# Performance work log

Hardware: AMD Instinct MI355X
Metric: run time of the kernel (lower is better)

## Reference

```python
import jax, jax.numpy as jnp
import numpy as np
from jax import lax

LATENT, HIDDEN, OUT = 64, 128, 64
B, T = 4096, 100


def setup_inputs() -> dict:
    key = jax.random.key(0)
    ks = jax.random.split(key, 12)
    s = lambda fan_in: 1.0 / np.sqrt(fan_in)
    u = lambda k, shape, fan_in: jax.random.uniform(k, shape, jnp.float32, -s(fan_in), s(fan_in))
    return {
        "z0": jax.random.normal(ks[0], (B, LATENT), jnp.float32),
        "t": jnp.arange(T, dtype=jnp.float32) * 0.01,  # increasing time grid
        "fc1_w": u(ks[1], (HIDDEN, LATENT), LATENT), "fc1_b": u(ks[2], (HIDDEN,), LATENT),
        "fc2_w": u(ks[3], (HIDDEN, HIDDEN), HIDDEN), "fc2_b": u(ks[4], (HIDDEN,), HIDDEN),
        "fc3_w": u(ks[5], (LATENT, HIDDEN), HIDDEN), "fc3_b": u(ks[6], (LATENT,), HIDDEN),
        "l2h_w": u(ks[7], (HIDDEN, LATENT), LATENT), "l2h_b": u(ks[8], (HIDDEN,), LATENT),
        "h2o_w": u(ks[9], (OUT, HIDDEN), HIDDEN), "h2o_b": u(ks[10], (OUT,), HIDDEN),
    }


def reference(z0, t, fc1_w, fc1_b, fc2_w, fc2_b, fc3_w, fc3_b, l2h_w, l2h_b, h2o_w, h2o_b):
    elu = jax.nn.elu

    def f(z):  # ODE_Func: fc1-elu-fc2-elu-fc3
        h = elu(z @ fc1_w.T + fc1_b)
        h = elu(h @ fc2_w.T + fc2_b)
        return h @ fc3_w.T + fc3_b

    dts = t[1:] - t[:-1]  # [T-1]

    def step(z, dt):  # fixed-step RK4
        k1 = f(z)
        k2 = f(z + 0.5 * dt * k1)
        k3 = f(z + 0.5 * dt * k2)
        k4 = f(z + dt * k3)
        zn = z + (dt / 6.0) * (k1 + 2.0 * k2 + 2.0 * k3 + k4)
        return zn, zn

    _, zs = lax.scan(step, z0, dts)          # [T-1, B, latent]
    pred_z = jnp.concatenate([z0[None], zs], axis=0)  # whole sequence [T, B, latent]
    # decode: h2o(relu(l2h(pred_z)))
    h = jax.nn.relu(pred_z @ l2h_w.T + l2h_b)
    return h @ h2o_w.T + h2o_b               # [T, B, out]
```

## Files before the change

### kernel.cpp

```cpp
#include <hip/hip_runtime.h>

typedef _Float16 f16;
typedef _Float16 f16x4 __attribute__((ext_vector_type(4)));
typedef _Float16 f16x8 __attribute__((ext_vector_type(8)));
typedef float    f32x4 __attribute__((ext_vector_type(4)));

#define MFMA16(a,b,c) __builtin_amdgcn_mfma_f32_16x16x32_f16((a),(b),(c),0,0,0)

#define LATENT 64
#define HIDDEN 128

__device__ __forceinline__ f16x8 load_afrag(const float* __restrict__ W, int K,
                                            int tile, int kf, int lane) {
  const int row = tile * 16 + (lane & 15);
  const int k0  = kf * 32 + (lane >> 4) * 8;
  const float* p = W + row * K + k0;
  f16x8 r;
#pragma unroll
  for (int j = 0; j < 8; ++j) r[j] = (f16)p[j];
  return r;
}

__device__ __forceinline__ f16x8 bfrag(const f16* buf, int rowb, int k0, int lane) {
  const int b  = lane & 15;
  const int kk = k0 + (lane >> 4) * 8;
  const int off = b * rowb + ((kk * 2) ^ ((b & 7) << 4));
  return *(const f16x8*)((const char*)buf + off);
}

__device__ __forceinline__ void dwrite(f16* buf, int rowb, int dbase, f32x4 v, int lane) {
  const int b = lane & 15;
  f16x4 h;
#pragma unroll
  for (int i = 0; i < 4; ++i) h[i] = (f16)v[i];
  const int off = b * rowb + ((dbase * 2) ^ ((b & 7) << 4));
  *(f16x4*)((char*)buf + off) = h;
}

__device__ __forceinline__ f32x4 elu4(f32x4 v) {
#pragma unroll
  for (int i = 0; i < 4; ++i) v[i] = v[i] > 0.f ? v[i] : (__expf(v[i]) - 1.f);
  return v;
}

__global__ __launch_bounds__(256, 1)
void node_rk4_kernel(const float* __restrict__ z0,   const float* __restrict__ tg,
                     const float* __restrict__ fc1w, const float* __restrict__ fc1b,
                     const float* __restrict__ fc2w, const float* __restrict__ fc2b,
                     const float* __restrict__ fc3w, const float* __restrict__ fc3b,
                     const float* __restrict__ l2hw, const float* __restrict__ l2hb,
                     const float* __restrict__ h2ow, const float* __restrict__ h2ob,
                     float* __restrict__ out, int Btot, int T) {
  __shared__ __align__(16) f16 xbuf[16 * 64];
  __shared__ __align__(16) f16 h1buf[16 * 128];
  __shared__ __align__(16) f16 h2buf[16 * 128];
  __shared__ __align__(16) float outst[16 * 64];

  const int tid  = threadIdx.x;
  const int lane = tid & 63;
  const int wv   = tid >> 6;
  const int grp  = lane >> 4;
  const int bcol = lane & 15;
  const int row0 = blockIdx.x * 16;
  const int dz   = wv * 16 + grp * 4;

  f16x8 a1[2][2], aL[2][2], a2[2][4], a3[4], aO[4];
#pragma unroll
  for (int ot = 0; ot < 2; ++ot) {
#pragma unroll
    for (int kf = 0; kf < 2; ++kf) {
      a1[ot][kf] = load_afrag(fc1w, 64, 2 * wv + ot, kf, lane);
      aL[ot][kf] = load_afrag(l2hw, 64, 2 * wv + ot, kf, lane);
    }
#pragma unroll
    for (int kf = 0; kf < 4; ++kf) a2[ot][kf] = load_afrag(fc2w, 128, 2 * wv + ot, kf, lane);
  }
#pragma unroll
  for (int kf = 0; kf < 4; ++kf) {
    a3[kf] = load_afrag(fc3w, 128, wv, kf, lane);
    aO[kf] = load_afrag(h2ow, 128, wv, kf, lane);
  }

  f32x4 b1[2], b2[2], bL[2], b3, bO;
#pragma unroll
  for (int ot = 0; ot < 2; ++ot) {
    const int d = (2 * wv + ot) * 16 + grp * 4;
    b1[ot] = *(const f32x4*)(fc1b + d);
    b2[ot] = *(const f32x4*)(fc2b + d);
    bL[ot] = *(const f32x4*)(l2hb + d);
  }
  b3 = *(const f32x4*)(fc3b + dz);
  bO = *(const f32x4*)(h2ob + dz);

  f32x4 z = *(const f32x4*)(z0 + (size_t)(row0 + bcol) * LATENT + dz);

  auto feval = [&]() -> f32x4 {
    const f16x8 v0 = bfrag(xbuf, 128, 0, lane);
    const f16x8 v1 = bfrag(xbuf, 128, 32, lane);
#pragma unroll
    for (int ot = 0; ot < 2; ++ot) {
      f32x4 d = {0.f, 0.f, 0.f, 0.f};
      d = MFMA16(a1[ot][0], v0, d);
      d = MFMA16(a1[ot][1], v1, d);
      d += b1[ot];
      d = elu4(d);
      dwrite(h1buf, 256, (2 * wv + ot) * 16 + grp * 4, d, lane);
    }
    __syncthreads();
#pragma unroll
    for (int ot = 0; ot < 2; ++ot) {
      f32x4 d = {0.f, 0.f, 0.f, 0.f};
#pragma unroll
      for (int kf = 0; kf < 4; ++kf) d = MFMA16(a2[ot][kf], bfrag(h1buf, 256, kf * 32, lane), d);
      d += b2[ot];
      d = elu4(d);
      dwrite(h2buf, 256, (2 * wv + ot) * 16 + grp * 4, d, lane);
    }
    __syncthreads();
    f32x4 d = {0.f, 0.f, 0.f, 0.f};
#pragma unroll
    for (int kf = 0; kf < 4; ++kf) d = MFMA16(a3[kf], bfrag(h2buf, 256, kf * 32, lane), d);
    d += b3;
    return d;
  };

  for (int s = 0;; ++s) {
    dwrite(xbuf, 128, dz, z, lane);
    __syncthreads();

    {
      const f16x8 x0 = bfrag(xbuf, 128, 0, lane);
      const f16x8 x1 = bfrag(xbuf, 128, 32, lane);
#pragma unroll
      for (int ot = 0; ot < 2; ++ot) {
        f32x4 d = {0.f, 0.f, 0.f, 0.f};
        d = MFMA16(aL[ot][0], x0, d);
        d = MFMA16(aL[ot][1], x1, d);
        d += bL[ot];
#pragma unroll
        for (int i = 0; i < 4; ++i) d[i] = fmaxf(d[i], 0.f);
        dwrite(h1buf, 256, (2 * wv + ot) * 16 + grp * 4, d, lane);
      }
      __syncthreads();
      f32x4 o = {0.f, 0.f, 0.f, 0.f};
#pragma unroll
      for (int kf = 0; kf < 4; ++kf) o = MFMA16(aO[kf], bfrag(h1buf, 256, kf * 32, lane), o);
      o += bO;
      const int off = bcol * 256 + ((dz * 4) ^ ((bcol & 7) << 4));
      *(f32x4*)((char*)outst + off) = o;
    }
    __syncthreads();
    {
      const int flat = tid * 4;
      const int b = flat >> 6;
      const int d = flat & 63;
      const int off = b * 256 + ((d * 4) ^ ((b & 7) << 4));
      f32x4 v = *(const f32x4*)((const char*)outst + off);
      *(f32x4*)(out + ((size_t)s * Btot + row0 + b) * LATENT + d) = v;
    }
    if (s == T - 1) break;

    const float dt = tg[s + 1] - tg[s];

    f32x4 k = feval();
    f32x4 acc = k;
    f32x4 xs;
#pragma unroll
    for (int i = 0; i < 4; ++i) xs[i] = z[i] + 0.5f * dt * k[i];
    dwrite(xbuf, 128, dz, xs, lane);
    __syncthreads();
    k = feval();
#pragma unroll
    for (int i = 0; i < 4; ++i) { acc[i] += 2.f * k[i]; xs[i] = z[i] + 0.5f * dt * k[i]; }
    dwrite(xbuf, 128, dz, xs, lane);
    __syncthreads();
    k = feval();
#pragma unroll
    for (int i = 0; i < 4; ++i) { acc[i] += 2.f * k[i]; xs[i] = z[i] + dt * k[i]; }
    dwrite(xbuf, 128, dz, xs, lane);
    __syncthreads();
    k = feval();
#pragma unroll
    for (int i = 0; i < 4; ++i) z[i] += (dt / 6.f) * (acc[i] + k[i]);
  }
}

extern "C" void kernel_launch(void* const* d_in, const int* in_sizes, int n_in,
                              void* d_out, int out_size, void* d_ws, size_t ws_size,
                              hipStream_t stream) {
  const float* z0   = (const float*)d_in[0];
  const float* tg   = (const float*)d_in[1];
  const float* fc1w = (const float*)d_in[2];
  const float* fc1b = (const float*)d_in[3];
  const float* fc2w = (const float*)d_in[4];
  const float* fc2b = (const float*)d_in[5];
  const float* fc3w = (const float*)d_in[6];
  const float* fc3b = (const float*)d_in[7];
  const float* l2hw = (const float*)d_in[8];
  const float* l2hb = (const float*)d_in[9];
  const float* h2ow = (const float*)d_in[10];
  const float* h2ob = (const float*)d_in[11];
  float* out = (float*)d_out;

  const int Btot = in_sizes[0] / LATENT;
  const int T    = in_sizes[1];

  dim3 grid(Btot / 16), block(256);
  node_rk4_kernel<<<grid, block, 0, stream>>>(z0, tg, fc1w, fc1b, fc2w, fc2b,
                                              fc3w, fc3b, l2hw, l2hb, h2ow, h2ob,
                                              out, Btot, T);
}
```

Before: 330.5 us.

## Warp-specialize: dedicated decoder waves overlap output decode with RK4 integration

```diff
diff --git a/kernel.cpp b/kernel.cpp
--- a/kernel.cpp
+++ b/kernel.cpp
@@ -43,7 +43,12 @@
   return v;
 }
 
-__global__ __launch_bounds__(256, 1)
+__device__ __forceinline__ void bar_raw() {
+  __builtin_amdgcn_s_barrier();
+  __builtin_amdgcn_sched_barrier(0);
+}
+
+__global__ __launch_bounds__(512, 2)
 void node_rk4_kernel(const float* __restrict__ z0,   const float* __restrict__ tg,
                      const float* __restrict__ fc1w, const float* __restrict__ fc1b,
                      const float* __restrict__ fc2w, const float* __restrict__ fc2b,
@@ -51,137 +56,156 @@
                      const float* __restrict__ l2hw, const float* __restrict__ l2hb,
                      const float* __restrict__ h2ow, const float* __restrict__ h2ob,
                      float* __restrict__ out, int Btot, int T) {
+  __shared__ __align__(16) f16 zhist[4][16 * 64];
   __shared__ __align__(16) f16 xbuf[16 * 64];
   __shared__ __align__(16) f16 h1buf[16 * 128];
   __shared__ __align__(16) f16 h2buf[16 * 128];
-  __shared__ __align__(16) float outst[16 * 64];
+  __shared__ __align__(16) f16 dch1[16 * 128];
 
   const int tid  = threadIdx.x;
   const int lane = tid & 63;
   const int wv   = tid >> 6;
+  const int iw   = wv & 3;
   const int grp  = lane >> 4;
   const int bcol = lane & 15;
   const int row0 = blockIdx.x * 16;
-  const int dz   = wv * 16 + grp * 4;
-
-  f16x8 a1[2][2], aL[2][2], a2[2][4], a3[4], aO[4];
-#pragma unroll
-  for (int ot = 0; ot < 2; ++ot) {
-#pragma unroll
-    for (int kf = 0; kf < 2; ++kf) {
-      a1[ot][kf] = load_afrag(fc1w, 64, 2 * wv + ot, kf, lane);
-      aL[ot][kf] = load_afrag(l2hw, 64, 2 * wv + ot, kf, lane);
-    }
-#pragma unroll
-    for (int kf = 0; kf < 4; ++kf) a2[ot][kf] = load_afrag(fc2w, 128, 2 * wv + ot, kf, lane);
-  }
-#pragma unroll
-  for (int kf = 0; kf < 4; ++kf) {
-    a3[kf] = load_afrag(fc3w, 128, wv, kf, lane);
-    aO[kf] = load_afrag(h2ow, 128, wv, kf, lane);
-  }
-
-  f32x4 b1[2], b2[2], bL[2], b3, bO;
-#pragma unroll
-  for (int ot = 0; ot < 2; ++ot) {
-    const int d = (2 * wv + ot) * 16 + grp * 4;
-    b1[ot] = *(const f32x4*)(fc1b + d);
-    b2[ot] = *(const f32x4*)(fc2b + d);
-    bL[ot] = *(const f32x4*)(l2hb + d);
-  }
-  b3 = *(const f32x4*)(fc3b + dz);
-  bO = *(const f32x4*)(h2ob + dz);
-
-  f32x4 z = *(const f32x4*)(z0 + (size_t)(row0 + bcol) * LATENT + dz);
-
-  auto feval = [&]() -> f32x4 {
-    const f16x8 v0 = bfrag(xbuf, 128, 0, lane);
-    const f16x8 v1 = bfrag(xbuf, 128, 32, lane);
+
+  if (wv < 4) {
+    f16x8 a1[2][2], a2[2][4], a3[4];
+    f32x4 b1[2], b2[2], b3;
 #pragma unroll
     for (int ot = 0; ot < 2; ++ot) {
-      f32x4 d = {0.f, 0.f, 0.f, 0.f};
-      d = MFMA16(a1[ot][0], v0, d);
-      d = MFMA16(a1[ot][1], v1, d);
-      d += b1[ot];
-      d = elu4(d);
-      dwrite(h1buf, 256, (2 * wv + ot) * 16 + grp * 4, d, lane);
-    }
-    __syncthreads();
-#pragma unroll
-    for (int ot = 0; ot < 2; ++ot) {
-      f32x4 d = {0.f, 0.f, 0.f, 0.f};
-#pragma unroll
-      for (int kf = 0; kf < 4; ++kf) d = MFMA16(a2[ot][kf], bfrag(h1buf, 256, kf * 32, lane), d);
-      d += b2[ot];
-      d = elu4(d);
-      dwrite(h2buf, 256, (2 * wv + ot) * 16 + grp * 4, d, lane);
-    }
-    __syncthreads();
-    f32x4 d = {0.f, 0.f, 0.f, 0.f};
-#pragma unroll
-    for (int kf = 0; kf < 4; ++kf) d = MFMA16(a3[kf], bfrag(h2buf, 256, kf * 32, lane), d);
-    d += b3;
-    return d;
-  };
-
-  for (int s = 0;; ++s) {
-    dwrite(xbuf, 128, dz, z, lane);
-    __syncthreads();
-
-    {
-      const f16x8 x0 = bfrag(xbuf, 128, 0, lane);
-      const f16x8 x1 = bfrag(xbuf, 128, 32, lane);
+#pragma unroll
+      for (int kf = 0; kf < 2; ++kf) a1[ot][kf] = load_afrag(fc1w, 64, 2 * iw + ot, kf, lane);
+#pragma unroll
+      for (int kf = 0; kf < 4; ++kf) a2[ot][kf] = load_afrag(fc2w, 128, 2 * iw + ot, kf, lane);
+      const int d = (2 * iw + ot) * 16 + grp * 4;
+      b1[ot] = *(const f32x4*)(fc1b + d);
+      b2[ot] = *(const f32x4*)(fc2b + d);
+    }
+#pragma unroll
+    for (int kf = 0; kf < 4; ++kf) a3[kf] = load_afrag(fc3w, 128, iw, kf, lane);
+    const int dz = iw * 16 + grp * 4;
+    b3 = *(const f32x4*)(fc3b + dz);
+
+    f32x4 z = *(const f32x4*)(z0 + (size_t)(row0 + bcol) * LATENT + dz);
+
+    auto feval = [&](const f16* xb) -> f32x4 {
+      const f16x8 v0 = bfrag(xb, 128, 0, lane);
+      const f16x8 v1 = bfrag(xb, 128, 32, lane);
 #pragma unroll
       for (int ot = 0; ot < 2; ++ot) {
         f32x4 d = {0.f, 0.f, 0.f, 0.f};
-        d = MFMA16(aL[ot][0], x0, d);
-        d = MFMA16(aL[ot][1], x1, d);
-        d += bL[ot];
-#pragma unroll
-        for (int i = 0; i < 4; ++i) d[i] = fmaxf(d[i], 0.f);
-        dwrite(h1buf, 256, (2 * wv + ot) * 16 + grp * 4, d, lane);
-      }
-      __syncthreads();
-      f32x4 o = {0.f, 0.f, 0.f, 0.f};
-#pragma unroll
-      for (int kf = 0; kf < 4; ++kf) o = MFMA16(aO[kf], bfrag(h1buf, 256, kf * 32, lane), o);
-      o += bO;
-      const int off = bcol * 256 + ((dz * 4) ^ ((bcol & 7) << 4));
-      *(f32x4*)((char*)outst + off) = o;
-    }
-    __syncthreads();
-    {
-      const int flat = tid * 4;
-      const int b = flat >> 6;
-      const int d = flat & 63;
-      const int off = b * 256 + ((d * 4) ^ ((b & 7) << 4));
-      f32x4 v = *(const f32x4*)((const char*)outst + off);
-      *(f32x4*)(out + ((size_t)s * Btot + row0 + b) * LATENT + d) = v;
-    }
-    if (s == T - 1) break;
-
-    const float dt = tg[s + 1] - tg[s];
-
-    f32x4 k = feval();
-    f32x4 acc = k;
-    f32x4 xs;
-#pragma unroll
-    for (int i = 0; i < 4; ++i) xs[i] = z[i] + 0.5f * dt * k[i];
-    dwrite(xbuf, 128, dz, xs, lane);
-    __syncthreads();
-    k = feval();
-#pragma unroll
-    for (int i = 0; i < 4; ++i) { acc[i] += 2.f * k[i]; xs[i] = z[i] + 0.5f * dt * k[i]; }
-    dwrite(xbuf, 128, dz, xs, lane);
-    __syncthreads();
-    k = feval();
-#pragma unroll
-    for (int i = 0; i < 4; ++i) { acc[i] += 2.f * k[i]; xs[i] = z[i] + dt * k[i]; }
-    dwrite(xbuf, 128, dz, xs, lane);
-    __syncthreads();
-    k = feval();
-#pragma unroll
-    for (int i = 0; i < 4; ++i) z[i] += (dt / 6.f) * (acc[i] + k[i]);
+        d = MFMA16(a1[ot][0], v0, d);
+        d = MFMA16(a1[ot][1], v1, d);
+        d += b1[ot];
+        d = elu4(d);
+        dwrite(h1buf, 256, (2 * iw + ot) * 16 + grp * 4, d, lane);
+      }
+      __syncthreads();
+      f16x8 h[4];
+#pragma unroll
+      for (int kf = 0; kf < 4; ++kf) h[kf] = bfrag(h1buf, 256, kf * 32, lane);
+#pragma unroll
+      for (int ot = 0; ot < 2; ++ot) {
+        f32x4 c0 = {0.f, 0.f, 0.f, 0.f}, c1 = {0.f, 0.f, 0.f, 0.f};
+        c0 = MFMA16(a2[ot][0], h[0], c0);
+        c0 = MFMA16(a2[ot][1], h[1], c0);
+        c1 = MFMA16(a2[ot][2], h[2], c1);
+        c1 = MFMA16(a2[ot][3], h[3], c1);
+        f32x4 d = c0 + c1 + b2[ot];
+        d = elu4(d);
+        dwrite(h2buf, 256, (2 * iw + ot) * 16 + grp * 4, d, lane);
+      }
+      __syncthreads();
+      f16x8 g[4];
+#pragma unroll
+      for (int kf = 0; kf < 4; ++kf) g[kf] = bfrag(h2buf, 256, kf * 32, lane);
+      f32x4 c0 = {0.f, 0.f, 0.f, 0.f}, c1 = {0.f, 0.f, 0.f, 0.f};
+      c0 = MFMA16(a3[0], g[0], c0);
+      c0 = MFMA16(a3[1], g[1], c0);
+      c1 = MFMA16(a3[2], g[2], c1);
+      c1 = MFMA16(a3[3], g[3], c1);
+      return c0 + c1 + b3;
+    };
+
+    for (int s = 0; s < T; ++s) {
+      dwrite(zhist[s & 3], 128, dz, z, lane);
+      __syncthreads();
+      if (s == T - 1) break;
+      const float dt = tg[s + 1] - tg[s];
+
+      f32x4 k = feval(zhist[s & 3]);
+      f32x4 acc = k, xs;
+#pragma unroll
+      for (int i = 0; i < 4; ++i) xs[i] = z[i] + 0.5f * dt * k[i];
+      dwrite(xbuf, 128, dz, xs, lane);
+      __syncthreads();
+      k = feval(xbuf);
+#pragma unroll
+      for (int i = 0; i < 4; ++i) { acc[i] += 2.f * k[i]; xs[i] = z[i] + 0.5f * dt * k[i]; }
+      dwrite(xbuf, 128, dz, xs, lane);
+      __syncthreads();
+      k = feval(xbuf);
+#pragma unroll
+      for (int i = 0; i < 4; ++i) { acc[i] += 2.f * k[i]; xs[i] = z[i] + dt * k[i]; }
+      dwrite(xbuf, 128, dz, xs, lane);
+      __syncthreads();
+      k = feval(xbuf);
+#pragma unroll
+      for (int i = 0; i < 4; ++i) z[i] += (dt / 6.f) * (acc[i] + k[i]);
+    }
+  } else {
+    f16x8 aL[8][2], aO[4][4];
+    f32x4 bLr[8], bOr[4];
+#pragma unroll
+    for (int ot = 0; ot < 8; ++ot) {
+      aL[ot][0] = load_afrag(l2hw, 64, ot, 0, lane);
+      aL[ot][1] = load_afrag(l2hw, 64, ot, 1, lane);
+      bLr[ot] = *(const f32x4*)(l2hb + ot * 16 + grp * 4);
+    }
+#pragma unroll
+    for (int t = 0; t < 4; ++t) {
+#pragma unroll
+      for (int kf = 0; kf < 4; ++kf) aO[t][kf] = load_afrag(h2ow, 128, t, kf, lane);
+      bOr[t] = *(const f32x4*)(h2ob + t * 16 + grp * 4);
+    }
+
+    for (int s = 0; s < T; ++s) {
+      bar_raw();
+      if ((s & 3) == iw) {
+        const f16* zb = zhist[s & 3];
+        const f16x8 zf0 = bfrag(zb, 128, 0, lane);
+        const f16x8 zf1 = bfrag(zb, 128, 32, lane);
+#pragma unroll
+        for (int ot = 0; ot < 8; ++ot) {
+          f32x4 d = {0.f, 0.f, 0.f, 0.f};
+          d = MFMA16(aL[ot][0], zf0, d);
+          d = MFMA16(aL[ot][1], zf1, d);
+          d += bLr[ot];
+#pragma unroll
+          for (int i = 0; i < 4; ++i) d[i] = fmaxf(d[i], 0.f);
+          dwrite(dch1, 256, ot * 16 + grp * 4, d, lane);
+        }
+        f16x8 h[4];
+#pragma unroll
+        for (int kf = 0; kf < 4; ++kf) h[kf] = bfrag(dch1, 256, kf * 32, lane);
+#pragma unroll
+        for (int t = 0; t < 4; ++t) {
+          f32x4 c0 = {0.f, 0.f, 0.f, 0.f}, c1 = {0.f, 0.f, 0.f, 0.f};
+          c0 = MFMA16(aO[t][0], h[0], c0);
+          c0 = MFMA16(aO[t][1], h[1], c0);
+          c1 = MFMA16(aO[t][2], h[2], c1);
+          c1 = MFMA16(aO[t][3], h[3], c1);
+          f32x4 o = c0 + c1 + bOr[t];
+          *(f32x4*)(out + ((size_t)s * Btot + row0 + bcol) * LATENT + t * 16 + grp * 4) = o;
+        }
+      }
+      if (s < T - 1) {
+#pragma unroll 1
+        for (int b2 = 0; b2 < 11; ++b2) bar_raw();
+      }
+    }
   }
 }
 
@@ -205,7 +229,7 @@
   const int Btot = in_sizes[0] / LATENT;
   const int T    = in_sizes[1];
 
-  dim3 grid(Btot / 16), block(256);
+  dim3 grid(Btot / 16), block(512);
   node_rk4_kernel<<<grid, block, 0, stream>>>(z0, tg, fc1w, fc1b, fc2w, fc2b,
                                               fc3w, fc3b, l2hw, l2hb, h2ow, h2ob,
                                               out, Btot, T);
```

Result: no change. 335.7 us (+1.6%).

## Halve rows per block to run two blocks per CU and shorten MFMA dependency chains

Applied to the files above, without the earlier changes.

```diff
diff --git a/kernel.cpp b/kernel.cpp
--- a/kernel.cpp
+++ b/kernel.cpp
@@ -3,12 +3,20 @@
 typedef _Float16 f16;
 typedef _Float16 f16x4 __attribute__((ext_vector_type(4)));
 typedef _Float16 f16x8 __attribute__((ext_vector_type(8)));
+typedef __fp16   h16x2 __attribute__((ext_vector_type(2)));
 typedef float    f32x4 __attribute__((ext_vector_type(4)));
+
+struct h16x2x2 { h16x2 lo, hi; };
 
 #define MFMA16(a,b,c) __builtin_amdgcn_mfma_f32_16x16x32_f16((a),(b),(c),0,0,0)
 
 #define LATENT 64
 #define HIDDEN 128
+#define ROWS   8
+
+__device__ __forceinline__ void bar_lds() {
+  asm volatile("s_waitcnt lgkmcnt(0)\n\ts_barrier" ::: "memory");
+}
 
 __device__ __forceinline__ f16x8 load_afrag(const float* __restrict__ W, int K,
                                             int tile, int kf, int lane) {
@@ -30,20 +38,24 @@
 
 __device__ __forceinline__ void dwrite(f16* buf, int rowb, int dbase, f32x4 v, int lane) {
   const int b = lane & 15;
-  f16x4 h;
-#pragma unroll
-  for (int i = 0; i < 4; ++i) h[i] = (f16)v[i];
+  h16x2x2 p;
+  p.lo = __builtin_amdgcn_cvt_pkrtz(v[0], v[1]);
+  p.hi = __builtin_amdgcn_cvt_pkrtz(v[2], v[3]);
+  const f16x4 h = __builtin_bit_cast(f16x4, p);
   const int off = b * rowb + ((dbase * 2) ^ ((b & 7) << 4));
   *(f16x4*)((char*)buf + off) = h;
 }
 
-__device__ __forceinline__ f32x4 elu4(f32x4 v) {
-#pragma unroll
-  for (int i = 0; i < 4; ++i) v[i] = v[i] > 0.f ? v[i] : (__expf(v[i]) - 1.f);
-  return v;
-}
-
-__global__ __launch_bounds__(256, 1)
+__device__ __forceinline__ f32x4 elu4(f32x4 d) {
+#pragma unroll
+  for (int i = 0; i < 4; ++i) {
+    const float e = __expf(d[i]) - 1.f;
+    d[i] = d[i] > 0.f ? d[i] : e;
+  }
+  return d;
+}
+
+__global__ __launch_bounds__(256, 2)
 void node_rk4_kernel(const float* __restrict__ z0,   const float* __restrict__ tg,
                      const float* __restrict__ fc1w, const float* __restrict__ fc1b,
                      const float* __restrict__ fc2w, const float* __restrict__ fc2b,
@@ -54,17 +66,17 @@
   __shared__ __align__(16) f16 xbuf[16 * 64];
   __shared__ __align__(16) f16 h1buf[16 * 128];
   __shared__ __align__(16) f16 h2buf[16 * 128];
-  __shared__ __align__(16) float outst[16 * 64];
 
   const int tid  = threadIdx.x;
   const int lane = tid & 63;
   const int wv   = tid >> 6;
   const int grp  = lane >> 4;
   const int bcol = lane & 15;
-  const int row0 = blockIdx.x * 16;
-  const int dz   = wv * 16 + grp * 4;
+  const int row0 = blockIdx.x * ROWS;
+  const f32x4 Z0 = {0.f, 0.f, 0.f, 0.f};
 
   f16x8 a1[2][2], aL[2][2], a2[2][4], a3[4], aO[4];
+  f32x4 b1[2], b2[2], bL[2], b3, bO;
 #pragma unroll
   for (int ot = 0; ot < 2; ++ot) {
 #pragma unroll
@@ -74,114 +86,114 @@
     }
 #pragma unroll
     for (int kf = 0; kf < 4; ++kf) a2[ot][kf] = load_afrag(fc2w, 128, 2 * wv + ot, kf, lane);
-  }
-#pragma unroll
-  for (int kf = 0; kf < 4; ++kf) {
-    a3[kf] = load_afrag(fc3w, 128, wv, kf, lane);
-    aO[kf] = load_afrag(h2ow, 128, wv, kf, lane);
-  }
-
-  f32x4 b1[2], b2[2], bL[2], b3, bO;
-#pragma unroll
-  for (int ot = 0; ot < 2; ++ot) {
     const int d = (2 * wv + ot) * 16 + grp * 4;
     b1[ot] = *(const f32x4*)(fc1b + d);
     b2[ot] = *(const f32x4*)(fc2b + d);
     bL[ot] = *(const f32x4*)(l2hb + d);
   }
+#pragma unroll
+  for (int kf = 0; kf < 4; ++kf) {
+    a3[kf] = load_afrag(fc3w, 128, wv, kf, lane);
+    aO[kf] = load_afrag(h2ow, 128, wv, kf, lane);
+  }
+  const int dz = wv * 16 + grp * 4;
   b3 = *(const f32x4*)(fc3b + dz);
   bO = *(const f32x4*)(h2ob + dz);
 
-  f32x4 z = *(const f32x4*)(z0 + (size_t)(row0 + bcol) * LATENT + dz);
+  const int rb = min(row0 + bcol, Btot - 1);
+  f32x4 z = *(const f32x4*)(z0 + (size_t)rb * LATENT + dz);
 
   auto feval = [&]() -> f32x4 {
     const f16x8 v0 = bfrag(xbuf, 128, 0, lane);
     const f16x8 v1 = bfrag(xbuf, 128, 32, lane);
 #pragma unroll
     for (int ot = 0; ot < 2; ++ot) {
-      f32x4 d = {0.f, 0.f, 0.f, 0.f};
-      d = MFMA16(a1[ot][0], v0, d);
+      f32x4 d = MFMA16(a1[ot][0], v0, b1[ot]);
       d = MFMA16(a1[ot][1], v1, d);
-      d += b1[ot];
       d = elu4(d);
       dwrite(h1buf, 256, (2 * wv + ot) * 16 + grp * 4, d, lane);
     }
-    __syncthreads();
+    bar_lds();
+    f16x8 h[4];
+#pragma unroll
+    for (int kf = 0; kf < 4; ++kf) h[kf] = bfrag(h1buf, 256, kf * 32, lane);
 #pragma unroll
     for (int ot = 0; ot < 2; ++ot) {
-      f32x4 d = {0.f, 0.f, 0.f, 0.f};
-#pragma unroll
-      for (int kf = 0; kf < 4; ++kf) d = MFMA16(a2[ot][kf], bfrag(h1buf, 256, kf * 32, lane), d);
-      d += b2[ot];
-      d = elu4(d);
+      f32x4 c0 = MFMA16(a2[ot][0], h[0], b2[ot]);
+      c0 = MFMA16(a2[ot][1], h[1], c0);
+      f32x4 c1 = MFMA16(a2[ot][2], h[2], Z0);
+      c1 = MFMA16(a2[ot][3], h[3], c1);
+      f32x4 d = elu4(c0 + c1);
       dwrite(h2buf, 256, (2 * wv + ot) * 16 + grp * 4, d, lane);
     }
-    __syncthreads();
-    f32x4 d = {0.f, 0.f, 0.f, 0.f};
-#pragma unroll
-    for (int kf = 0; kf < 4; ++kf) d = MFMA16(a3[kf], bfrag(h2buf, 256, kf * 32, lane), d);
-    d += b3;
-    return d;
+    bar_lds();
+    f16x8 g[4];
+#pragma unroll
+    for (int kf = 0; kf < 4; ++kf) g[kf] = bfrag(h2buf, 256, kf * 32, lane);
+    f32x4 c0 = MFMA16(a3[0], g[0], b3);
+    c0 = MFMA16(a3[1], g[1], c0);
+    f32x4 c1 = MFMA16(a3[2], g[2], Z0);
+    c1 = MFMA16(a3[3], g[3], c1);
+    return c0 + c1;
   };
 
+  float t_cur = tg[0];
+  float t_nxt = tg[1];
   for (int s = 0;; ++s) {
     dwrite(xbuf, 128, dz, z, lane);
-    __syncthreads();
+    bar_lds();
 
     {
       const f16x8 x0 = bfrag(xbuf, 128, 0, lane);
       const f16x8 x1 = bfrag(xbuf, 128, 32, lane);
 #pragma unroll
       for (int ot = 0; ot < 2; ++ot) {
-        f32x4 d = {0.f, 0.f, 0.f, 0.f};
-        d = MFMA16(aL[ot][0], x0, d);
+        f32x4 d = MFMA16(aL[ot][0], x0, bL[ot]);
         d = MFMA16(aL[ot][1], x1, d);
-        d += bL[ot];
 #pragma unroll
         for (int i = 0; i < 4; ++i) d[i] = fmaxf(d[i], 0.f);
         dwrite(h1buf, 256, (2 * wv + ot) * 16 + grp * 4, d, lane);
       }
-      __syncthreads();
-      f32x4 o = {0.f, 0.f, 0.f, 0.f};
-#pragma unroll
-      for (int kf = 0; kf < 4; ++kf) o = MFMA16(aO[kf], bfrag(h1buf, 256, kf * 32, lane), o);
-      o += bO;
-      const int off = bcol * 256 + ((dz * 4) ^ ((bcol & 7) << 4));
-      *(f32x4*)((char*)outst + off) = o;
-    }
-    __syncthreads();
-    {
-      const int flat = tid * 4;
-      const int b = flat >> 6;
-      const int d = flat & 63;
-      const int off = b * 256 + ((d * 4) ^ ((b & 7) << 4));
-      f32x4 v = *(const f32x4*)((const char*)outst + off);
-      *(f32x4*)(out + ((size_t)s * Btot + row0 + b) * LATENT + d) = v;
+      bar_lds();
+      f16x8 h[4];
+#pragma unroll
+      for (int kf = 0; kf < 4; ++kf) h[kf] = bfrag(h1buf, 256, kf * 32, lane);
+      bar_lds();
+      f32x4 c0 = MFMA16(aO[0], h[0], bO);
+      c0 = MFMA16(aO[1], h[1], c0);
+      f32x4 c1 = MFMA16(aO[2], h[2], Z0);
+      c1 = MFMA16(aO[3], h[3], c1);
+      f32x4 o = c0 + c1;
+      if (bcol < ROWS)
+        *(f32x4*)(out + ((size_t)s * Btot + row0 + bcol) * LATENT + dz) = o;
     }
     if (s == T - 1) break;
 
-    const float dt = tg[s + 1] - tg[s];
+    const float t_fut = tg[s + 2 < T ? s + 2 : T - 1];
+    const float dt = t_nxt - t_cur;
 
     f32x4 k = feval();
-    f32x4 acc = k;
-    f32x4 xs;
+    f32x4 acc = k, xs;
 #pragma unroll
     for (int i = 0; i < 4; ++i) xs[i] = z[i] + 0.5f * dt * k[i];
     dwrite(xbuf, 128, dz, xs, lane);
-    __syncthreads();
+    bar_lds();
     k = feval();
 #pragma unroll
     for (int i = 0; i < 4; ++i) { acc[i] += 2.f * k[i]; xs[i] = z[i] + 0.5f * dt * k[i]; }
     dwrite(xbuf, 128, dz, xs, lane);
-    __syncthreads();
+    bar_lds();
     k = feval();
 #pragma unroll
     for (int i = 0; i < 4; ++i) { acc[i] += 2.f * k[i]; xs[i] = z[i] + dt * k[i]; }
     dwrite(xbuf, 128, dz, xs, lane);
-    __syncthreads();
+    bar_lds();
     k = feval();
 #pragma unroll
     for (int i = 0; i < 4; ++i) z[i] += (dt / 6.f) * (acc[i] + k[i]);
+
+    t_cur = t_nxt;
+    t_nxt = t_fut;
   }
 }
 
@@ -205,7 +217,7 @@
   const int Btot = in_sizes[0] / LATENT;
   const int T    = in_sizes[1];
 
-  dim3 grid(Btot / 16), block(256);
+  dim3 grid((Btot + ROWS - 1) / ROWS), block(256);
   node_rk4_kernel<<<grid, block, 0, stream>>>(z0, tg, fc1w, fc1b, fc2w, fc2b,
                                               fc3w, fc3b, l2hw, l2hb, h2ow, h2ob,
                                               out, Btot, T);
```

New measurement: 390.2 us. 1.18x slower.
